# Performance work log

Measured on AMD Instinct MI355X. Metric: run time of the kernel, lower is better.

Reference implementation:

```python
import jax, jax.numpy as jnp
import numpy as np

HEAD_DIM = 256
ROPE_THETA = 1000000.0
EPS = 1e-6


def rmsnorm(x, w):
    # torch.nn.RMSNorm: x / sqrt(mean(x^2) + eps) * w, over last dim
    var = jnp.mean(jnp.square(x), axis=-1, keepdims=True)
    return x * jax.lax.rsqrt(var + EPS) * w


def apply_rope(x):
    # x: [b, h, L, head_dim]; rotate-half-split RoPE as in the source
    L, hd = x.shape[-2], x.shape[-1]
    half = hd // 2
    pos = jnp.arange(L, dtype=x.dtype)
    idx = jnp.arange(half, dtype=x.dtype)
    inv_freq = 1.0 / (ROPE_THETA ** (2.0 * idx / hd))
    freqs = pos[:, None] * inv_freq[None, :]          # [L, half]
    cos = jnp.cos(freqs)[None, None]                  # [1,1,L,half]
    sin = jnp.sin(freqs)[None, None]
    x1, x2 = x[..., :half], x[..., half:]
    return jnp.concatenate([x1 * cos - x2 * sin, x1 * sin + x2 * cos], axis=-1)


def setup_inputs() -> dict:
    key = jax.random.key(0)
    ks = jax.random.split(key, 7)
    B, L, D = 2, 2048, 2048
    H, HD = 8, HEAD_DIM
    s = lambda fan_in: 1.0 / np.sqrt(fan_in)
    return {
        "x": jax.random.normal(ks[0], (B, L, D), jnp.float32),
        "q_proj": jax.random.normal(ks[1], (H * HD, D), jnp.float32) * s(D),
        "k_proj": jax.random.normal(ks[2], (HD, D), jnp.float32) * s(D),
        "v_proj": jax.random.normal(ks[3], (HD, D), jnp.float32) * s(D),
        "o_proj": jax.random.normal(ks[4], (D, H * HD), jnp.float32) * s(H * HD),
        "q_norm": jnp.ones((HD,), jnp.float32),
        "k_norm": jnp.ones((HD,), jnp.float32),
    }


def reference(x, q_proj, k_proj, v_proj, o_proj, q_norm, k_norm):
    B, L, D = x.shape
    HD = k_proj.shape[0]
    H = q_proj.shape[0] // HD

    # projections (Linear weight is [out, in])
    k = rmsnorm(x @ k_proj.T, k_norm)                 # [B, L, HD]
    q = rmsnorm((x @ q_proj.T).reshape(B, L, H, HD), q_norm)
    v = x @ v_proj.T                                  # [B, L, HD]

    q = q.transpose(0, 2, 1, 3)                       # [B, H, L, HD]
    k = k[:, None]                                    # [B, 1, L, HD] (MQA)
    v = v[:, None]

    q = apply_rope(q)
    k = apply_rope(k)

    scores = jnp.matmul(q, jnp.swapaxes(k, -1, -2)) / jnp.sqrt(
        jnp.asarray(256.0, x.dtype))                  # [B, H, L, L]
    causal = jnp.tril(jnp.ones((L, L), bool))
    scores = jnp.where(causal, scores, -jnp.inf)
    w = jax.nn.softmax(scores, axis=-1)
    ctx = jnp.matmul(w, v)                            # [B, H, L, HD]
    ctx = ctx.transpose(0, 2, 1, 3).reshape(B, L, H * HD)
    return ctx @ o_proj.T
```

## Files before the change

kernel.cpp:

```cpp
#include <hip/hip_runtime.h>
#include <hip/hip_bf16.h>
#include <stdint.h>

typedef __bf16 bf16;
typedef bf16 bf16x8 __attribute__((ext_vector_type(8)));
typedef float f32x4 __attribute__((ext_vector_type(4)));

__device__ __forceinline__ bf16x8 load8(const float* p) {
    const f32x4 lo = *(const f32x4*)p;
    const f32x4 hi = *(const f32x4*)(p + 4);
    bf16x8 v;
#pragma unroll
    for (int r = 0; r < 4; ++r) { v[r] = (bf16)lo[r]; v[4 + r] = (bf16)hi[r]; }
    return v;
}
__device__ __forceinline__ bf16x8 load8(const bf16* p) {
    return *(const bf16x8*)p;
}

__device__ __forceinline__ void gload16(const bf16* g, bf16* l) {
    __builtin_amdgcn_global_load_lds((const __attribute__((address_space(1))) void*)g,
                                     (__attribute__((address_space(3))) void*)l, 16, 0, 0);
}

__global__ __launch_bounds__(256) void cvt_bf16(const float* __restrict__ src,
                                                bf16* __restrict__ dst, int n8) {
    int idx = blockIdx.x * 256 + threadIdx.x;
    const int stride = gridDim.x * 256;
    for (; idx < n8; idx += stride) {
        const f32x4 lo = *(const f32x4*)(src + (size_t)idx * 8);
        const f32x4 hi = *(const f32x4*)(src + (size_t)idx * 8 + 4);
        bf16x8 v;
#pragma unroll
        for (int r = 0; r < 4; ++r) { v[r] = (bf16)lo[r]; v[4 + r] = (bf16)hi[r]; }
        *(bf16x8*)(dst + (size_t)idx * 8) = v;
    }
}

template <typename AT, typename BT, typename CT>
__global__ __launch_bounds__(256) void gemm_bt(const AT* __restrict__ A,
                                               const BT* __restrict__ B,
                                               CT* __restrict__ C,
                                               int M, int N, int K) {
    __shared__ __align__(16) bf16 As[128 * 32];
    __shared__ __align__(16) bf16 Bs[128 * 32];
    const int tid  = threadIdx.x;
    const int wave = tid >> 6, lane = tid & 63;
    const int quad = lane >> 4, l16 = lane & 15;
    const int m0 = blockIdx.y * 128, n0 = blockIdx.x * 128;
    const int wr = (wave >> 1) * 64, wc = (wave & 1) * 64;

    const int srow = wave * 32 + (lane >> 2);
    const int scol = (lane & 3) * 8;
    const AT* Ag = A + (size_t)(m0 + srow) * K + scol;
    const BT* Bg = B + (size_t)(n0 + srow) * K + scol;
    bf16* Asw = &As[srow * 32 + scol];
    bf16* Bsw = &Bs[srow * 32 + scol];

    f32x4 acc[4][4] = {};

    for (int k0 = 0; k0 < K; k0 += 32) {
        const bf16x8 av0 = load8(Ag + k0);
        const bf16x8 av1 = load8(Ag + k0 + (size_t)16 * K);
        const bf16x8 bv0 = load8(Bg + k0);
        const bf16x8 bv1 = load8(Bg + k0 + (size_t)16 * K);
        __syncthreads();
        *(bf16x8*)(Asw)           = av0;
        *(bf16x8*)(Asw + 16 * 32) = av1;
        *(bf16x8*)(Bsw)           = bv0;
        *(bf16x8*)(Bsw + 16 * 32) = bv1;
        __syncthreads();

        bf16x8 a[4], b[4];
#pragma unroll
        for (int i = 0; i < 4; ++i)
            a[i] = *(const bf16x8*)&As[(wr + i * 16 + l16) * 32 + quad * 8];
#pragma unroll
        for (int j = 0; j < 4; ++j)
            b[j] = *(const bf16x8*)&Bs[(wc + j * 16 + l16) * 32 + quad * 8];
#pragma unroll
        for (int i = 0; i < 4; ++i)
#pragma unroll
            for (int j = 0; j < 4; ++j)
                acc[i][j] = __builtin_amdgcn_mfma_f32_16x16x32_bf16(a[i], b[j], acc[i][j], 0, 0, 0);
    }

#pragma unroll
    for (int i = 0; i < 4; ++i)
#pragma unroll
        for (int j = 0; j < 4; ++j) {
            const int row = m0 + wr + i * 16 + quad * 4;
            const int col = n0 + wc + j * 16 + l16;
#pragma unroll
            for (int r = 0; r < 4; ++r)
                C[(size_t)(row + r) * N + col] = (CT)acc[i][j][r];
        }
}

template <typename CT>
__global__ __launch_bounds__(256) void gemm_bb(const bf16* __restrict__ A,
                                               const bf16* __restrict__ B,
                                               CT* __restrict__ C,
                                               int M, int N, int K) {
    __shared__ __align__(16) bf16 As[128 * 32];
    __shared__ __align__(16) bf16 Bs[128 * 32];
    const int tid  = threadIdx.x;
    const int wave = tid >> 6, lane = tid & 63;
    const int quad = lane >> 4, l16 = lane & 15;
    const int m0 = blockIdx.y * 128, n0 = blockIdx.x * 128;
    const int wr = (wave >> 1) * 64, wc = (wave & 1) * 64;

    const int srow = tid >> 2, scol = (tid & 3) * 8;
    const bf16* Ag = A + (size_t)(m0 + srow) * K + scol;
    const bf16* Bg = B + (size_t)(n0 + srow) * K + scol;
    bf16* Adst = As + wave * 512;
    bf16* Bdst = Bs + wave * 512;

    f32x4 acc[4][4] = {};

    for (int k0 = 0; k0 < K; k0 += 32) {
        __syncthreads();
        gload16(Ag + k0, Adst);
        gload16(Ag + k0 + (size_t)64 * K, Adst + 2048);
        gload16(Bg + k0, Bdst);
        gload16(Bg + k0 + (size_t)64 * K, Bdst + 2048);
        __syncthreads();

        bf16x8 a[4], b[4];
#pragma unroll
        for (int i = 0; i < 4; ++i)
            a[i] = *(const bf16x8*)&As[(wr + i * 16 + l16) * 32 + quad * 8];
#pragma unroll
        for (int j = 0; j < 4; ++j)
            b[j] = *(const bf16x8*)&Bs[(wc + j * 16 + l16) * 32 + quad * 8];
#pragma unroll
        for (int i = 0; i < 4; ++i)
#pragma unroll
            for (int j = 0; j < 4; ++j)
                acc[i][j] = __builtin_amdgcn_mfma_f32_16x16x32_bf16(a[i], b[j], acc[i][j], 0, 0, 0);
    }

#pragma unroll
    for (int i = 0; i < 4; ++i)
#pragma unroll
        for (int j = 0; j < 4; ++j) {
            const int row = m0 + wr + i * 16 + quad * 4;
            const int col = n0 + wc + j * 16 + l16;
#pragma unroll
            for (int r = 0; r < 4; ++r)
                C[(size_t)(row + r) * N + col] = (CT)acc[i][j][r];
        }
}

__global__ __launch_bounds__(256) void gemm_qkv(const bf16* __restrict__ A,
                                                const bf16* __restrict__ W,
                                                bf16* __restrict__ Cq,
                                                bf16* __restrict__ Ck,
                                                bf16* __restrict__ Cv,
                                                int M, int K) {
    __shared__ __align__(16) bf16 As[128 * 32];
    __shared__ __align__(16) bf16 Bs[128 * 32];
    const int tid  = threadIdx.x;
    const int wave = tid >> 6, lane = tid & 63;
    const int quad = lane >> 4, l16 = lane & 15;
    const int m0 = blockIdx.y * 128, n0 = blockIdx.x * 128;
    const int wr = (wave >> 1) * 64, wc = (wave & 1) * 64;

    const int srow = tid >> 2, scol = (tid & 3) * 8;
    const bf16* Ag = A + (size_t)(m0 + srow) * K + scol;
    const bf16* Bg = W + (size_t)(n0 + srow) * K + scol;
    bf16* Adst = As + wave * 512;
    bf16* Bdst = Bs + wave * 512;

    f32x4 acc[4][4] = {};

    for (int k0 = 0; k0 < K; k0 += 32) {
        __syncthreads();
        gload16(Ag + k0, Adst);
        gload16(Ag + k0 + (size_t)64 * K, Adst + 2048);
        gload16(Bg + k0, Bdst);
        gload16(Bg + k0 + (size_t)64 * K, Bdst + 2048);
        __syncthreads();

        bf16x8 a[4], b[4];
#pragma unroll
        for (int i = 0; i < 4; ++i)
            a[i] = *(const bf16x8*)&As[(wr + i * 16 + l16) * 32 + quad * 8];
#pragma unroll
        for (int j = 0; j < 4; ++j)
            b[j] = *(const bf16x8*)&Bs[(wc + j * 16 + l16) * 32 + quad * 8];
#pragma unroll
        for (int i = 0; i < 4; ++i)
#pragma unroll
            for (int j = 0; j < 4; ++j)
                acc[i][j] = __builtin_amdgcn_mfma_f32_16x16x32_bf16(a[i], b[j], acc[i][j], 0, 0, 0);
    }

    bf16* cb; int cw, coff;
    if (n0 < 2048)      { cb = Cq; cw = 2048; coff = 0; }
    else if (n0 < 2304) { cb = Ck; cw = 256;  coff = 2048; }
    else                { cb = Cv; cw = 256;  coff = 2304; }

#pragma unroll
    for (int i = 0; i < 4; ++i)
#pragma unroll
        for (int j = 0; j < 4; ++j) {
            const int row = m0 + wr + i * 16 + quad * 4;
            const int col = n0 + wc + j * 16 + l16 - coff;
#pragma unroll
            for (int r = 0; r < 4; ++r)
                cb[(size_t)(row + r) * cw + col] = (bf16)acc[i][j][r];
        }
}

__global__ __launch_bounds__(256) void norm_rope(bf16* __restrict__ x,
                                                 const float* __restrict__ w,
                                                 int L, int div) {
    const int row = blockIdx.x;
    const int t = threadIdx.x;
    const size_t base = (size_t)row * 256;

    const float v = (float)x[base + t];
    float ss = v * v;
#pragma unroll
    for (int off = 32; off >= 1; off >>= 1) ss += __shfl_xor(ss, off);

    __shared__ float wsum[4];
    __shared__ float buf[256];
    const int wave = t >> 6, lane = t & 63;
    if (lane == 0) wsum[wave] = ss;
    __syncthreads();
    const float var = (wsum[0] + wsum[1] + wsum[2] + wsum[3]) * (1.0f / 256.0f);
    const float inv = rsqrtf(var + 1e-6f);
    buf[t] = v * inv * w[t];
    __syncthreads();

    const int pos = (row / div) % L;
    const int i = t & 127;
    const float freq = (float)pos * exp2f(-(float)i * (19.93156857f / 128.0f));
    const float c = cosf(freq), s = sinf(freq);
    const float x1 = buf[i], x2 = buf[i + 128];
    const float out = (t < 128) ? (x1 * c - x2 * s) : (x1 * s + x2 * c);
    x[base + t] = (bf16)out;
}

__global__ __launch_bounds__(256) void transpose_v(const bf16* __restrict__ V,
                                                   bf16* __restrict__ Vt, int L) {
    __shared__ bf16 tile[32][33];
    const int b = blockIdx.z;
    const int l0 = blockIdx.x * 32, d0 = blockIdx.y * 32;
    const int tx = threadIdx.x & 31, ty = threadIdx.x >> 5;
#pragma unroll
    for (int i = 0; i < 32; i += 8)
        tile[ty + i][tx] = V[((size_t)b * L + l0 + ty + i) * 256 + d0 + tx];
    __syncthreads();
#pragma unroll
    for (int i = 0; i < 32; i += 8)
        Vt[((size_t)b * 256 + d0 + ty + i) * L + l0 + tx] = tile[tx][ty + i];
}

__device__ __forceinline__ int kswz(int r, int c) { return r * 256 + (c ^ ((r & 7) << 3)); }
__device__ __forceinline__ int vswz(int r, int c) { return r * 64  + (c ^ ((r & 7) << 3)); }

template <int SPLIT>
__global__ __launch_bounds__(256, 2) void flash_attn(const bf16* __restrict__ Q,
                                                     const bf16* __restrict__ K,
                                                     const bf16* __restrict__ Vt,
                                                     bf16* __restrict__ Ctx,
                                                     float* __restrict__ P0,
                                                     float* __restrict__ P1,
                                                     float* __restrict__ ML0,
                                                     float* __restrict__ ML1, int L) {
    constexpr int H = 8, HD = 256;
    extern __shared__ __align__(16) bf16 smem[];
    bf16* Ks = smem;
    bf16* Vs = Ks + 64 * 256;
    bf16* Ps = Vs + 256 * 64;

    const int z = blockIdx.x, h = blockIdx.y;
    const int b    = SPLIT ? ((int)blockIdx.z >> 1) : (int)blockIdx.z;
    const int half = SPLIT ? ((int)blockIdx.z & 1) : 0;
    const int tid = threadIdx.x;
    const int wave = tid >> 6, lane = tid & 63;
    const int quad = lane >> 4, l16 = lane & 15;
    const int nqt = L / 64;

    const bf16* Kb = K + (size_t)b * L * HD;
    const bf16* Vb = Vt + (size_t)b * HD * L;
    bf16* Pw = Ps + wave * 16 * 64;

    const int krow = tid >> 5, kcol = (tid & 31) * 8;
    const int vrow = tid >> 3, vcol = (tid & 7) * 8;
    const int kcs = kcol ^ ((krow & 7) << 3);
    const int vcs = vcol ^ ((vrow & 7) << 3);
    bf16* kdst = Ks + wave * 512;
    bf16* vdst = Vs + wave * 512;

    for (int pass = 0; pass < 2; ++pass) {
        const int qt = pass ? z : (nqt - 1 - z);
        const int q0 = qt * 64 + wave * 16;
        const int s  = qt + 1;
        const int c0 = (s + 1) >> 1;
        const int kt0 = (SPLIT && half) ? c0 : 0;
        const int cnt = SPLIT ? (half ? s - c0 : c0) : s;

        bf16x8 qf[8];
        {
            const bf16* qbase = Q + ((size_t)(b * L + q0 + l16) * H + h) * HD + quad * 8;
#pragma unroll
            for (int kc = 0; kc < 8; ++kc) qf[kc] = *(const bf16x8*)(qbase + kc * 32);
        }

        f32x4 Oacc[16] = {};
        float mrow[4], lrow[4];
#pragma unroll
        for (int r = 0; r < 4; ++r) { mrow[r] = -1e30f; lrow[r] = 0.0f; }

        __syncthreads();
        if (cnt > 0) {
            const int kv0 = kt0 * 64;
#pragma unroll
            for (int i = 0; i < 8; ++i)
                gload16(Kb + (size_t)(kv0 + i * 8 + krow) * HD + kcs, kdst + i * 2048);
#pragma unroll
            for (int i = 0; i < 8; ++i)
                gload16(Vb + (size_t)(i * 32 + vrow) * L + kv0 + vcs, vdst + i * 2048);
        }
        __syncthreads();

        for (int it = 0; it < cnt; ++it) {
            const int kt = kt0 + it;
            const int kv0 = kt * 64;
            const bool more = (it + 1 < cnt);

            f32x4 S[4];
#pragma unroll
            for (int nt = 0; nt < 4; ++nt) {
                f32x4 slo = {0.f, 0.f, 0.f, 0.f}, shi = {0.f, 0.f, 0.f, 0.f};
                const int krw = nt * 16 + l16;
#pragma unroll
                for (int kc = 0; kc < 4; ++kc)
                    slo = __builtin_amdgcn_mfma_f32_16x16x32_bf16(qf[kc], *(const bf16x8*)&Ks[kswz(krw, quad * 8 + kc * 32)], slo, 0, 0, 0);
#pragma unroll
                for (int kc = 4; kc < 8; ++kc)
                    shi = __builtin_amdgcn_mfma_f32_16x16x32_bf16(qf[kc], *(const bf16x8*)&Ks[kswz(krw, quad * 8 + kc * 32)], shi, 0, 0, 0);
                S[nt] = slo + shi;
            }

            float rowmax[4] = {-1e30f, -1e30f, -1e30f, -1e30f};
            const bool diag = (kt == qt);
#pragma unroll
            for (int nt = 0; nt < 4; ++nt) {
                const int col = kv0 + nt * 16 + l16;
#pragma unroll
                for (int r = 0; r < 4; ++r) {
                    float sv = S[nt][r] * 0.0625f;
                    if (diag && col > q0 + quad * 4 + r) sv = -1e30f;
                    S[nt][r] = sv;
                    rowmax[r] = fmaxf(rowmax[r], sv);
                }
            }
#pragma unroll
            for (int off = 1; off < 16; off <<= 1)
#pragma unroll
                for (int r = 0; r < 4; ++r)
                    rowmax[r] = fmaxf(rowmax[r], __shfl_xor(rowmax[r], off));

            float alpha[4], rsum[4];
#pragma unroll
            for (int r = 0; r < 4; ++r) {
                const float mnew = fmaxf(mrow[r], rowmax[r]);
                alpha[r] = __expf(mrow[r] - mnew);
                mrow[r] = mnew;
                rsum[r] = 0.0f;
            }
#pragma unroll
            for (int nt = 0; nt < 4; ++nt)
#pragma unroll
                for (int r = 0; r < 4; ++r) {
                    const float p = __expf(S[nt][r] - mrow[r]);
                    rsum[r] += p;
                    Pw[vswz(quad * 4 + r, nt * 16 + l16)] = (bf16)p;
                }
#pragma unroll
            for (int off = 1; off < 16; off <<= 1)
#pragma unroll
                for (int r = 0; r < 4; ++r) rsum[r] += __shfl_xor(rsum[r], off);
#pragma unroll
            for (int r = 0; r < 4; ++r) lrow[r] = lrow[r] * alpha[r] + rsum[r];

#pragma unroll
            for (int nt = 0; nt < 16; ++nt)
#pragma unroll
                for (int r = 0; r < 4; ++r) Oacc[nt][r] *= alpha[r];

            bf16x8 pf[2];
#pragma unroll
            for (int ks = 0; ks < 2; ++ks)
                pf[ks] = *(const bf16x8*)&Pw[vswz(l16, ks * 32 + quad * 8)];
#pragma unroll
            for (int nt = 0; nt < 16; ++nt) {
                const int vrw = nt * 16 + l16;
                f32x4 o = Oacc[nt];
#pragma unroll
                for (int ks = 0; ks < 2; ++ks)
                    o = __builtin_amdgcn_mfma_f32_16x16x32_bf16(pf[ks], *(const bf16x8*)&Vs[vswz(vrw, ks * 32 + quad * 8)], o, 0, 0, 0);
                Oacc[nt] = o;
            }

            __syncthreads();
            if (more) {
                const int nv0 = kv0 + 64;
#pragma unroll
                for (int i = 0; i < 8; ++i)
                    gload16(Kb + (size_t)(nv0 + i * 8 + krow) * HD + kcs, kdst + i * 2048);
#pragma unroll
                for (int i = 0; i < 8; ++i)
                    gload16(Vb + (size_t)(i * 32 + vrow) * L + nv0 + vcs, vdst + i * 2048);
                __syncthreads();
            }
        }

        if (SPLIT) {
            float* Pd  = half ? P1 : P0;
            float* MLd = half ? ML1 : ML0;
            const size_t rowbase = (((size_t)b * H + h) * nqt + qt) * 64 + wave * 16;
            float* prow = Pd + rowbase * 256;
#pragma unroll
            for (int nt = 0; nt < 16; ++nt)
#pragma unroll
                for (int r = 0; r < 4; ++r)
                    prow[(size_t)(quad * 4 + r) * 256 + nt * 16 + l16] = Oacc[nt][r];
            if (l16 == 0) {
#pragma unroll
                for (int r = 0; r < 4; ++r) {
                    const size_t rr = rowbase + quad * 4 + r;
                    MLd[rr * 2 + 0] = mrow[r];
                    MLd[rr * 2 + 1] = lrow[r];
                }
            }
        } else {
            bf16* obase = Ctx + ((size_t)(b * L + q0) * H + h) * HD;
#pragma unroll
            for (int nt = 0; nt < 16; ++nt)
#pragma unroll
                for (int r = 0; r < 4; ++r) {
                    const float val = Oacc[nt][r] / lrow[r];
                    obase[(size_t)(quad * 4 + r) * (H * HD) + nt * 16 + l16] = (bf16)val;
                }
        }
    }
}

__global__ __launch_bounds__(256) void merge_partials(const float* __restrict__ P0,
                                                      const float* __restrict__ P1,
                                                      const float* __restrict__ ML0,
                                                      const float* __restrict__ ML1,
                                                      bf16* __restrict__ Ctx, int L) {
    constexpr int H = 8, HD = 256;
    const int qt = blockIdx.x, h = blockIdx.y, b = blockIdx.z;
    const int nqt = L / 64;
    const int t = threadIdx.x;
    const size_t rowbase = (((size_t)b * H + h) * nqt + qt) * 64;
    const int rlo = t >> 6;
    const int d = (t & 63) * 4;
#pragma unroll
    for (int it = 0; it < 16; ++it) {
        const int r = it * 4 + rlo;
        const size_t rr = rowbase + r;
        const float m0 = ML0[rr * 2], l0 = ML0[rr * 2 + 1];
        const float m1 = ML1[rr * 2], l1 = ML1[rr * 2 + 1];
        const float mn = fmaxf(m0, m1);
        const float a0 = __expf(m0 - mn), a1 = __expf(m1 - mn);
        const float linv = 1.0f / (l0 * a0 + l1 * a1);
        const f32x4 o0 = *(const f32x4*)&P0[rr * 256 + d];
        const f32x4 o1 = *(const f32x4*)&P1[rr * 256 + d];
        bf16* op = Ctx + ((size_t)(b * L + qt * 64 + r) * H + h) * HD + d;
#pragma unroll
        for (int j = 0; j < 4; ++j) op[j] = (bf16)((o0[j] * a0 + o1[j] * a1) * linv);
    }
}

extern "C" void kernel_launch(void* const* d_in, const int* in_sizes, int n_in,
                              void* d_out, int out_size, void* d_ws, size_t ws_size,
                              hipStream_t stream) {
    const float* x      = (const float*)d_in[0];
    const float* q_proj = (const float*)d_in[1];
    const float* k_proj = (const float*)d_in[2];
    const float* v_proj = (const float*)d_in[3];
    const float* o_proj = (const float*)d_in[4];
    const float* q_norm = (const float*)d_in[5];
    const float* k_norm = (const float*)d_in[6];
    float* out = (float*)d_out;

    constexpr int B = 2, L = 2048, D = 2048, H = 8, HD = 256;
    constexpr int M = B * L;
    constexpr int NQT = L / 64;
    constexpr int NQKV = D + 2 * HD;
    constexpr int FLASH_LDS = (64 * 256 + 256 * 64 + 4 * 16 * 64) * 2;

    static bool attr_set = false;
    if (!attr_set) {
        (void)hipFuncSetAttribute((const void*)flash_attn<0>,
                                  hipFuncAttributeMaxDynamicSharedMemorySize, FLASH_LDS);
        (void)hipFuncSetAttribute((const void*)flash_attn<1>,
                                  hipFuncAttributeMaxDynamicSharedMemorySize, FLASH_LDS);
        attr_set = true;
    }

    bf16* Qw  = (bf16*)d_ws;
    bf16* Kw  = Qw  + (size_t)M * D;
    bf16* Vw  = Kw  + (size_t)M * HD;
    bf16* Vtw = Vw  + (size_t)M * HD;
    bf16* Ctx = Vtw + (size_t)M * HD;

    char* region = (char*)(Ctx + (size_t)M * D);
    bf16* Xb   = (bf16*)region;
    bf16* Wqkv = Xb + (size_t)M * D;
    constexpr size_t PELEMS  = (size_t)B * H * NQT * 64 * 256;
    constexpr size_t MLELEMS = (size_t)B * H * NQT * 64 * 2;
    float* P0  = (float*)region;
    float* P1  = P0 + PELEMS;
    float* ML0 = P1 + PELEMS;
    float* ML1 = ML0 + MLELEMS;
    bf16*  Ob  = (bf16*)region;
    const size_t ws_needed = (size_t)((char*)(ML1 + MLELEMS) - (char*)d_ws);

    if (ws_size >= ws_needed) {
        cvt_bf16<<<2048, 256, 0, stream>>>(x, Xb, M * D / 8);
        cvt_bf16<<<2048, 256, 0, stream>>>(q_proj, Wqkv, D * D / 8);
        cvt_bf16<<<256, 256, 0, stream>>>(k_proj, Wqkv + (size_t)D * D, HD * D / 8);
        cvt_bf16<<<256, 256, 0, stream>>>(v_proj, Wqkv + (size_t)(D + HD) * D, HD * D / 8);
        gemm_qkv<<<dim3(NQKV / 128, M / 128), 256, 0, stream>>>(Xb, Wqkv, Qw, Kw, Vw, M, D);
        norm_rope<<<M * H, 256, 0, stream>>>(Qw, q_norm, L, H);
        norm_rope<<<M, 256, 0, stream>>>(Kw, k_norm, L, 1);
        transpose_v<<<dim3(L / 32, HD / 32, B), 256, 0, stream>>>(Vw, Vtw, L);
        flash_attn<1><<<dim3(L / 128, H, B * 2), 256, FLASH_LDS, stream>>>(Qw, Kw, Vtw, Ctx,
                                                                           P0, P1, ML0, ML1, L);
        merge_partials<<<dim3(NQT, H, B), 256, 0, stream>>>(P0, P1, ML0, ML1, Ctx, L);
        cvt_bf16<<<2048, 256, 0, stream>>>(o_proj, Ob, D * D / 8);
        gemm_bb<float><<<dim3(D / 128, M / 128), 256, 0, stream>>>(Ctx, Ob, out, M, D, D);
    } else {
        gemm_bt<float, float, bf16><<<dim3(D / 128, M / 128), 256, 0, stream>>>(x, q_proj, Qw, M, D, D);
        gemm_bt<float, float, bf16><<<dim3(HD / 128, M / 128), 256, 0, stream>>>(x, k_proj, Kw, M, HD, D);
        gemm_bt<float, float, bf16><<<dim3(HD / 128, M / 128), 256, 0, stream>>>(x, v_proj, Vw, M, HD, D);
        norm_rope<<<M * H, 256, 0, stream>>>(Qw, q_norm, L, H);
        norm_rope<<<M, 256, 0, stream>>>(Kw, k_norm, L, 1);
        transpose_v<<<dim3(L / 32, HD / 32, B), 256, 0, stream>>>(Vw, Vtw, L);
        flash_attn<0><<<dim3(L / 128, H, B), 256, FLASH_LDS, stream>>>(Qw, Kw, Vtw, Ctx,
                                                                       P0, P1, ML0, ML1, L);
        gemm_bt<bf16, float, float><<<dim3(D / 128, M / 128), 256, 0, stream>>>(Ctx, o_proj, out, M, D, D);
    }
}
```

Measured before the change: 359.0 us.

## Prefetch next K tile early in flash attention and fuse preprocessing launches

In the attention loop, the next K tile is now loaded into shared memory right after the QK^T MFMAs, so it overlaps the softmax and PV work. The V tile is still loaded at the end of the iteration, and one barrier per iteration is dropped. Separately, the four fp32-to-bf16 conversions become one launch, as do the Q and K norm+RoPE kernels, cutting launch overhead. The extra mid-loop barrier and the reordered loads add synchronisation risk, and correctness depends on the barrier implicitly waiting for the async LDS loads.

```diff
diff --git a/kernel.cpp b/kernel.cpp
--- a/kernel.cpp
+++ b/kernel.cpp
@@ -34,6 +34,31 @@
 #pragma unroll
         for (int r = 0; r < 4; ++r) { v[r] = (bf16)lo[r]; v[4 + r] = (bf16)hi[r]; }
         *(bf16x8*)(dst + (size_t)idx * 8) = v;
+    }
+}
+
+__global__ __launch_bounds__(256) void cvt_qkvx(const float* __restrict__ x,
+                                                const float* __restrict__ q,
+                                                const float* __restrict__ k,
+                                                const float* __restrict__ v,
+                                                bf16* __restrict__ dst,
+                                                int nx8, int nq8, int nk8, int nv8) {
+    const int total = nx8 + nq8 + nk8 + nv8;
+    int idx = blockIdx.x * 256 + threadIdx.x;
+    const int stride = gridDim.x * 256;
+    for (; idx < total; idx += stride) {
+        const float* s;
+        int off;
+        if (idx < nx8)                   { s = x; off = idx; }
+        else if (idx < nx8 + nq8)        { s = q; off = idx - nx8; }
+        else if (idx < nx8 + nq8 + nk8)  { s = k; off = idx - nx8 - nq8; }
+        else                             { s = v; off = idx - nx8 - nq8 - nk8; }
+        const f32x4 lo = *(const f32x4*)(s + (size_t)off * 8);
+        const f32x4 hi = *(const f32x4*)(s + (size_t)off * 8 + 4);
+        bf16x8 o;
+#pragma unroll
+        for (int r = 0; r < 4; ++r) { o[r] = (bf16)lo[r]; o[4 + r] = (bf16)hi[r]; }
+        *(bf16x8*)(dst + (size_t)idx * 8) = o;
     }
 }
 
@@ -213,13 +238,10 @@
         }
 }
 
-__global__ __launch_bounds__(256) void norm_rope(bf16* __restrict__ x,
-                                                 const float* __restrict__ w,
-                                                 int L, int div) {
-    const int row = blockIdx.x;
-    const int t = threadIdx.x;
-    const size_t base = (size_t)row * 256;
-
+__device__ __forceinline__ void norm_rope_body(bf16* __restrict__ x,
+                                               const float* __restrict__ w,
+                                               int rid, int L, int div, int t) {
+    const size_t base = (size_t)rid * 256;
     const float v = (float)x[base + t];
     float ss = v * v;
 #pragma unroll
@@ -235,13 +257,29 @@
     buf[t] = v * inv * w[t];
     __syncthreads();
 
-    const int pos = (row / div) % L;
+    const int pos = (rid / div) % L;
     const int i = t & 127;
     const float freq = (float)pos * exp2f(-(float)i * (19.93156857f / 128.0f));
     const float c = cosf(freq), s = sinf(freq);
     const float x1 = buf[i], x2 = buf[i + 128];
     const float out = (t < 128) ? (x1 * c - x2 * s) : (x1 * s + x2 * c);
     x[base + t] = (bf16)out;
+}
+
+__global__ __launch_bounds__(256) void norm_rope(bf16* __restrict__ x,
+                                                 const float* __restrict__ w,
+                                                 int L, int div) {
+    norm_rope_body(x, w, blockIdx.x, L, div, threadIdx.x);
+}
+
+__global__ __launch_bounds__(256) void norm_rope2(bf16* __restrict__ Q,
+                                                  bf16* __restrict__ K,
+                                                  const float* __restrict__ qw,
+                                                  const float* __restrict__ kw,
+                                                  int L, int MH) {
+    const int row = blockIdx.x;
+    if (row < MH) norm_rope_body(Q, qw, row, L, 8, threadIdx.x);
+    else          norm_rope_body(K, kw, row - MH, L, 1, threadIdx.x);
 }
 
 __global__ __launch_bounds__(256) void transpose_v(const bf16* __restrict__ V,
@@ -331,6 +369,7 @@
         for (int it = 0; it < cnt; ++it) {
             const int kt = kt0 + it;
             const int kv0 = kt * 64;
+            const int nv0 = kv0 + 64;
             const bool more = (it + 1 < cnt);
 
             f32x4 S[4];
@@ -345,6 +384,13 @@
                 for (int kc = 4; kc < 8; ++kc)
                     shi = __builtin_amdgcn_mfma_f32_16x16x32_bf16(qf[kc], *(const bf16x8*)&Ks[kswz(krw, quad * 8 + kc * 32)], shi, 0, 0, 0);
                 S[nt] = slo + shi;
+            }
+
+            __syncthreads();
+            if (more) {
+#pragma unroll
+                for (int i = 0; i < 8; ++i)
+                    gload16(Kb + (size_t)(nv0 + i * 8 + krow) * HD + kcs, kdst + i * 2048);
             }
 
             float rowmax[4] = {-1e30f, -1e30f, -1e30f, -1e30f};
@@ -410,14 +456,9 @@
 
             __syncthreads();
             if (more) {
-                const int nv0 = kv0 + 64;
-#pragma unroll
-                for (int i = 0; i < 8; ++i)
-                    gload16(Kb + (size_t)(nv0 + i * 8 + krow) * HD + kcs, kdst + i * 2048);
 #pragma unroll
                 for (int i = 0; i < 8; ++i)
                     gload16(Vb + (size_t)(i * 32 + vrow) * L + nv0 + vcs, vdst + i * 2048);
-                __syncthreads();
             }
         }
 
@@ -527,13 +568,10 @@
     const size_t ws_needed = (size_t)((char*)(ML1 + MLELEMS) - (char*)d_ws);
 
     if (ws_size >= ws_needed) {
-        cvt_bf16<<<2048, 256, 0, stream>>>(x, Xb, M * D / 8);
-        cvt_bf16<<<2048, 256, 0, stream>>>(q_proj, Wqkv, D * D / 8);
-        cvt_bf16<<<256, 256, 0, stream>>>(k_proj, Wqkv + (size_t)D * D, HD * D / 8);
-        cvt_bf16<<<256, 256, 0, stream>>>(v_proj, Wqkv + (size_t)(D + HD) * D, HD * D / 8);
+        cvt_qkvx<<<2048, 256, 0, stream>>>(x, q_proj, k_proj, v_proj, Xb,
+                                           M * D / 8, D * D / 8, HD * D / 8, HD * D / 8);
         gemm_qkv<<<dim3(NQKV / 128, M / 128), 256, 0, stream>>>(Xb, Wqkv, Qw, Kw, Vw, M, D);
-        norm_rope<<<M * H, 256, 0, stream>>>(Qw, q_norm, L, H);
-        norm_rope<<<M, 256, 0, stream>>>(Kw, k_norm, L, 1);
+        norm_rope2<<<M * H + M, 256, 0, stream>>>(Qw, Kw, q_norm, k_norm, L, M * H);
         transpose_v<<<dim3(L / 32, HD / 32, B), 256, 0, stream>>>(Vw, Vtw, L);
         flash_attn<1><<<dim3(L / 128, H, B * 2), 256, FLASH_LDS, stream>>>(Qw, Kw, Vtw, Ctx,
                                                                            P0, P1, ML0, ML1, L);
```

After: 354.6 us. Within noise of the previous version (-1.2%).
